# Performance work log

Measured on AMD Instinct MI355X. Metric: run time of the kernel, lower is better.

The kernel has to match this reference:

```python
import jax, jax.numpy as jnp
import numpy as np

EPS = 1e-5

def _conv1x1(x, w, b=None):
    # x: (B, Cin, H, W), w: (Cout, Cin) -> (B, Cout, H, W)
    y = jnp.einsum('bchw,oc->bohw', x, w)
    if b is not None:
        y = y + b[None, :, None, None]
    return y

def setup_inputs() -> dict:
    key = jax.random.key(0)
    ks = jax.random.split(key, 14)
    B, C, I = 4, 256, 128
    Ha = Wa = 64
    Hd = Wd = 128
    s = 0.05
    return {
        'detect':  jax.random.normal(ks[0], (B, C, Hd, Wd), jnp.float32),
        'aim':     jax.random.normal(ks[1], (B, C, Ha, Wa), jnp.float32),
        'g_w':     jax.random.normal(ks[2], (I, C), jnp.float32) * s,
        'g_b':     jax.random.normal(ks[3], (I,), jnp.float32) * s,
        'theta_w': jax.random.normal(ks[4], (I, C), jnp.float32) * s,
        'theta_b': jax.random.normal(ks[5], (I,), jnp.float32) * s,
        'phi_w':   jax.random.normal(ks[6], (I, C), jnp.float32) * s,
        'phi_b':   jax.random.normal(ks[7], (I,), jnp.float32) * s,
        'q_w':     jax.random.normal(ks[8], (C, I), jnp.float32) * s,
        'q_b':     jax.random.normal(ks[9], (C,), jnp.float32) * s,
        'bn_gamma': jax.random.normal(ks[10], (C,), jnp.float32),
        'bn_beta':  jax.random.normal(ks[11], (C,), jnp.float32),
        'bn_mean':  jax.random.normal(ks[12], (C,), jnp.float32),
        'bn_var':   jax.random.uniform(ks[13], (C,), jnp.float32) + 0.5,
    }

def reference(detect, aim, g_w, g_b, theta_w, theta_b, phi_w, phi_b,
              q_w, q_b, bn_gamma, bn_beta, bn_mean, bn_var):
    B, C, Hd, Wd = detect.shape
    _, _, Ha, Wa = aim.shape
    Na = Ha * Wa
    Nd = Hd * Wd
    I = g_w.shape[0]

    # 1x1 conv projections, flattened to token sequences
    a_g   = _conv1x1(aim, g_w, g_b).reshape(B, I, Na)        # g(aim)
    th_a  = _conv1x1(aim, theta_w, theta_b).reshape(B, I, Na)
    ph_d  = _conv1x1(detect, phi_w, phi_b).reshape(B, I, Nd)
    # (d_x = g(detect) is dead code in the original forward; omitted)

    # f = theta_x @ phi_x : (B, Na, Nd); permuted -> (B, Nd, Na); N = Na
    f = jnp.einsum('bia,bid->bad', th_a, ph_d)               # (B, Na, Nd)
    inv_n = jnp.float32(1.0 / Na)
    # non_det = (f^T / Na) @ a_x : (B, Nd, I) -> permute -> (B, I, Nd)
    non = jnp.einsum('bad,bia->bid', f * inv_n, a_g)         # (B, I, Nd)
    non = non.reshape(B, I, Hd, Wd)

    # Q: 1x1 conv (I -> C) + BatchNorm (inference mode, running stats)
    y = _conv1x1(non, q_w, q_b)
    inv_std = jax.lax.rsqrt(bn_var + EPS)
    y = (y - bn_mean[None, :, None, None]) * (bn_gamma * inv_std)[None, :, None, None] \
        + bn_beta[None, :, None, None]

    return y + detect
```

## Files before the change

### kernel.cpp

```cpp
#include <hip/hip_runtime.h>

constexpr int BB   = 4;
constexpr int CCH  = 256;
constexpr int IDIM = 128;
constexpr int NAa  = 4096;
constexpr int NDd  = 16384;
constexpr int PAD  = 320;
constexpr float NAinv = 1.0f / 4096.0f;

typedef __bf16 bf16x8 __attribute__((ext_vector_type(8)));
typedef float  f32x4  __attribute__((ext_vector_type(4)));

__device__ inline unsigned short f2bfu(float f) {
    unsigned u = __float_as_uint(f);
    u += 0x7FFFu + ((u >> 16) & 1u);
    return (unsigned short)(u >> 16);
}

__global__ __launch_bounds__(256) void k_prep(const float* __restrict__ qw,
                                              const float* __restrict__ gw,
                                              const float* __restrict__ gb,
                                              const float* __restrict__ thw,
                                              const float* __restrict__ thb,
                                              const float* __restrict__ phw,
                                              const float* __restrict__ phb,
                                              unsigned short* __restrict__ Ph,
                                              unsigned short* __restrict__ Rt) {
    const int idx = blockIdx.x * 256 + threadIdx.x;
    if (idx < CCH * PAD) {
        const int o = idx / PAD, c = idx - o * PAD;
        float acc = 0.f;
        if (c <= 256) {
            for (int i = 0; i < IDIM; ++i)
                acc += qw[o * IDIM + i] * ((c < 256) ? gw[i * CCH + c] : gb[i]);
        }
        Ph[idx] = f2bfu(acc);
    } else {
        const int id2 = idx - CCH * PAD;
        const int c2 = id2 / PAD, k = id2 - c2 * PAD;
        float acc = 0.f;
        if (k <= 256 && c2 <= 256) {
            for (int i = 0; i < IDIM; ++i) {
                const float av = (k < 256) ? thw[i * CCH + k] : thb[i];
                const float bv = (c2 < 256) ? phw[i * CCH + c2] : phb[i];
                acc += av * bv;
            }
        }
        Rt[id2] = f2bfu(acc);
    }
}

__device__ inline int at_idx(int row, int col) {
    return row * 320 + ((((col >> 3) ^ (row & 7)) << 3) | (col & 7));
}

__global__ __launch_bounds__(256) void k_V(const float* __restrict__ aim,
                                           const unsigned short* __restrict__ Ph,
                                           const unsigned short* __restrict__ Rt,
                                           unsigned short* __restrict__ V1,
                                           unsigned short* __restrict__ V2) {
    const int b = blockIdx.y, n0 = blockIdx.x * 64;
    const float* A = aim + (long)b * CCH * NAa;
    const int t = threadIdx.x, w = t >> 6, lane = t & 63, quad = lane >> 4, l16 = lane & 15;
    __shared__ __align__(16) unsigned short At[64 * 320];

    #pragma unroll 4
    for (int rep = 0; rep < 64; ++rep) {
        const int c = rep * 4 + w;
        At[at_idx(lane, c)] = f2bfu(A[(long)c * NAa + n0 + lane]);
    }
    {
        const int nn = t & 63, k0 = 256 + (t >> 6) * 16;
        #pragma unroll
        for (int k = k0; k < k0 + 16; ++k)
            At[at_idx(nn, k)] = (k == 256) ? (unsigned short)0x3F80u : (unsigned short)0u;
    }
    __syncthreads();

    for (int task = w; task < 9; task += 4) {
        const unsigned short* src;
        unsigned short* dst;
        int m0;
        if (task < 4) { m0 = task * 64;       src = Ph; dst = V1 + (long)b * CCH * NAa; }
        else          { m0 = (task - 4) * 64; src = Rt; dst = V2 + (long)b * PAD * NAa; }
        f32x4 acc[4][4] = {};
        for (int kt = 0; kt < PAD; kt += 32) {
            bf16x8 af[4], bfr[4];
            #pragma unroll
            for (int i = 0; i < 4; ++i)
                af[i] = *(const bf16x8*)(src + (long)(m0 + i * 16 + l16) * PAD + kt + quad * 8);
            #pragma unroll
            for (int j = 0; j < 4; ++j)
                bfr[j] = *(const bf16x8*)&At[at_idx(j * 16 + l16, kt + quad * 8)];
            #pragma unroll
            for (int i = 0; i < 4; ++i)
                #pragma unroll
                for (int j = 0; j < 4; ++j)
                    acc[i][j] = __builtin_amdgcn_mfma_f32_16x16x32_bf16(af[i], bfr[j], acc[i][j], 0, 0, 0);
        }
        #pragma unroll
        for (int i = 0; i < 4; ++i)
            #pragma unroll
            for (int j = 0; j < 4; ++j)
                #pragma unroll
                for (int reg = 0; reg < 4; ++reg)
                    dst[(long)(m0 + i * 16 + quad * 4 + reg) * NAa + n0 + j * 16 + l16] = f2bfu(acc[i][j][reg]);
    }
}

__global__ __launch_bounds__(256) void k_W(const unsigned short* __restrict__ V1,
                                           const unsigned short* __restrict__ V2,
                                           const float* __restrict__ qb,
                                           const float* __restrict__ gamma,
                                           const float* __restrict__ beta,
                                           const float* __restrict__ mean,
                                           const float* __restrict__ var,
                                           unsigned short* __restrict__ W5u,
                                           float* __restrict__ b5) {
    const int b = blockIdx.z;
    const int n0 = blockIdx.x * 64, m0 = blockIdx.y * 64;
    const unsigned short* Va = V1 + (long)b * CCH * NAa;
    const unsigned short* Vb = V2 + (long)b * PAD * NAa;
    const int t = threadIdx.x, w = t >> 6, lane = t & 63, quad = lane >> 4, l16 = lane & 15;
    __shared__ float sred[3 * 4096];

    f32x4 acc[4][4] = {};
    for (int ks = 0; ks < 32; ++ks) {
        const int k = w * 1024 + ks * 32 + quad * 8;
        bf16x8 af[4], bfr[4];
        #pragma unroll
        for (int i = 0; i < 4; ++i) af[i]  = *(const bf16x8*)(Va + (long)(m0 + i * 16 + l16) * NAa + k);
        #pragma unroll
        for (int j = 0; j < 4; ++j) bfr[j] = *(const bf16x8*)(Vb + (long)(n0 + j * 16 + l16) * NAa + k);
        #pragma unroll
        for (int i = 0; i < 4; ++i)
            #pragma unroll
            for (int j = 0; j < 4; ++j)
                acc[i][j] = __builtin_amdgcn_mfma_f32_16x16x32_bf16(af[i], bfr[j], acc[i][j], 0, 0, 0);
    }
    if (w > 0) {
        #pragma unroll
        for (int i = 0; i < 4; ++i)
            #pragma unroll
            for (int j = 0; j < 4; ++j)
                #pragma unroll
                for (int reg = 0; reg < 4; ++reg)
                    sred[(w - 1) * 4096 + ((i * 4 + j) * 4 + reg) * 64 + lane] = acc[i][j][reg];
    }
    __syncthreads();
    if (w == 0) {
        #pragma unroll
        for (int i = 0; i < 4; ++i)
            #pragma unroll
            for (int j = 0; j < 4; ++j)
                #pragma unroll
                for (int reg = 0; reg < 4; ++reg) {
                    float v = acc[i][j][reg];
                    #pragma unroll
                    for (int rg = 0; rg < 3; ++rg)
                        v += sred[rg * 4096 + ((i * 4 + j) * 4 + reg) * 64 + lane];
                    acc[i][j][reg] = v;
                }
        #pragma unroll
        for (int i = 0; i < 4; ++i) {
            #pragma unroll
            for (int reg = 0; reg < 4; ++reg) {
                const int o = m0 + i * 16 + quad * 4 + reg;
                const float s = gamma[o] * rsqrtf(var[o] + 1e-5f);
                #pragma unroll
                for (int j = 0; j < 4; ++j) {
                    const int c2 = n0 + j * 16 + l16;
                    const float val = acc[i][j][reg] * s * NAinv;
                    if (c2 < CCH)
                        W5u[((long)b * CCH + o) * CCH + c2] = f2bfu(val + (o == c2 ? 1.0f : 0.0f));
                    else if (c2 == CCH)
                        b5[b * CCH + o] = val + s * (qb[o] - mean[o]) + beta[o];
                }
            }
        }
    }
}

__global__ __launch_bounds__(512) void k_final(const float* __restrict__ D0,
                                               const unsigned short* __restrict__ W5u,
                                               const float* __restrict__ b5,
                                               float* __restrict__ out) {
    const int z = blockIdx.z;
    const int nb = blockIdx.x * 128;
    const float* D = D0 + (long)z * CCH * NDd;
    float* O = out + (long)z * CCH * NDd;
    const unsigned short* W = W5u + (long)z * CCH * CCH;
    const int t = threadIdx.x, wv = t >> 6, lane = t & 63, quad = lane >> 4, l16 = lane & 15;
    const int mw = (wv >> 1) * 64, nw = (wv & 1) * 64;
    const int r2 = t >> 4, g = t & 15;
    const bool st = (t < 256);
    __shared__ __align__(16) unsigned short lb[2][128][40];

    f32x4 xa[4], xb[4];
    bf16x8 af[2][4], bfr[4];

    auto load_tile = [&](f32x4* x, int kt) {
        const float* base = D + (long)(kt + 2 * r2) * NDd + nb + 8 * g;
        x[0] = *(const f32x4*)(base);
        x[1] = *(const f32x4*)(base + NDd);
        x[2] = *(const f32x4*)(base + 4);
        x[3] = *(const f32x4*)(base + NDd + 4);
    };
    auto write_tile = [&](int buf, const f32x4* x) {
        #pragma unroll
        for (int e2 = 0; e2 < 2; ++e2)
            #pragma unroll
            for (int c = 0; c < 4; ++c) {
                const int n = 8 * g + 4 * e2 + c;
                const int p = ((n & 7) << 4) + (n >> 3);
                const unsigned v = (unsigned)f2bfu(x[2 * e2][c]) |
                                   ((unsigned)f2bfu(x[2 * e2 + 1][c]) << 16);
                *(unsigned*)&lb[buf][p][2 * r2] = v;
            }
    };
    auto loadW = [&](bf16x8* a, int kt) {
        #pragma unroll
        for (int i = 0; i < 4; ++i)
            a[i] = *(const bf16x8*)(W + (long)(mw + i * 16 + l16) * CCH + kt + quad * 8);
    };

    int pj[4];
    #pragma unroll
    for (int j = 0; j < 4; ++j) {
        const int n = nw + j * 16 + l16;
        pj[j] = ((n & 7) << 4) + (n >> 3);
    }

    f32x4 acc[4][4] = {};
    if (st) { load_tile(xa, 0); load_tile(xb, 32); }
    loadW(af[0], 0);
    if (st) { write_tile(0, xa); load_tile(xa, 64); }
    #pragma unroll
    for (int it = 0; it < 8; ++it) {
        __syncthreads();
        const int kt = it * 32;
        #pragma unroll
        for (int j = 0; j < 4; ++j)
            bfr[j] = *(const bf16x8*)&lb[it & 1][pj[j]][quad * 8];
        #pragma unroll
        for (int i = 0; i < 4; ++i)
            #pragma unroll
            for (int j = 0; j < 4; ++j)
                acc[i][j] = __builtin_amdgcn_mfma_f32_16x16x32_bf16(af[it & 1][i], bfr[j], acc[i][j], 0, 0, 0);
        if (it < 7) {
            loadW(af[(it + 1) & 1], kt + 32);
            if (st) {
                write_tile((it + 1) & 1, (it & 1) ? xa : xb);
                if (it < 5) load_tile((it & 1) ? xa : xb, (it + 3) * 32);
            }
        }
    }
    #pragma unroll
    for (int i = 0; i < 4; ++i) {
        float bv[4];
        #pragma unroll
        for (int reg = 0; reg < 4; ++reg)
            bv[reg] = b5[z * CCH + mw + i * 16 + quad * 4 + reg];
        #pragma unroll
        for (int j = 0; j < 4; ++j) {
            const int n = nb + nw + j * 16 + l16;
            #pragma unroll
            for (int reg = 0; reg < 4; ++reg)
                O[(long)(mw + i * 16 + quad * 4 + reg) * NDd + n] = acc[i][j][reg] + bv[reg];
        }
    }
}

extern "C" void kernel_launch(void* const* d_in, const int* in_sizes, int n_in,
                              void* d_out, int out_size, void* d_ws, size_t ws_size,
                              hipStream_t stream) {
    const float* detect = (const float*)d_in[0];
    const float* aim    = (const float*)d_in[1];
    const float* g_w    = (const float*)d_in[2];
    const float* g_b    = (const float*)d_in[3];
    const float* th_w   = (const float*)d_in[4];
    const float* th_b   = (const float*)d_in[5];
    const float* phi_w  = (const float*)d_in[6];
    const float* phi_b  = (const float*)d_in[7];
    const float* q_w    = (const float*)d_in[8];
    const float* q_b    = (const float*)d_in[9];
    const float* gamma  = (const float*)d_in[10];
    const float* beta   = (const float*)d_in[11];
    const float* mean   = (const float*)d_in[12];
    const float* var    = (const float*)d_in[13];
    float* out = (float*)d_out;

    unsigned short* us = (unsigned short*)d_ws;
    unsigned short* V1u = us;
    unsigned short* V2u = V1u + 4194304;
    unsigned short* Phat_u  = V2u + 5242880;
    unsigned short* RhatT_u = Phat_u + 81920;
    unsigned short* W5u     = RhatT_u + 102400;
    float* b5 = (float*)(W5u + 262144);

    k_prep<<<dim3((CCH * PAD + PAD * PAD) / 256), dim3(256), 0, stream>>>(
        q_w, g_w, g_b, th_w, th_b, phi_w, phi_b, Phat_u, RhatT_u);
    k_V<<<dim3(NAa / 64, BB), dim3(256), 0, stream>>>(aim, Phat_u, RhatT_u, V1u, V2u);
    k_W<<<dim3(5, 4, BB), dim3(256), 0, stream>>>(V1u, V2u, q_b, gamma, beta, mean, var, W5u, b5);
    k_final<<<dim3(NDd / 128, 1, BB), dim3(512), 0, stream>>>(detect, W5u, b5, out);
}
```

Baseline: 240.2 us.

## Reassociate attention weight build through aim Gram matrix and fuse prep kernels

Replaces the per-batch projections V1/V2 over all Na tokens (then their contraction) with a Gram matrix S = aim·aimᵀ (256x256 per batch) plus aim row sums. The fused weight matrix is then rebuilt from small products Ph·S·Rtᵀ with rank-one bias corrections. Weight preparation, Gram and row-sum computation are merged into one launch. This removes the large bf16 intermediate writes and reads and one kernel launch. The cost is a serial small-GEMM chain in k2 that runs on only 16 blocks, and different bf16 rounding points.

```diff
diff --git a/kernel.cpp b/kernel.cpp
--- a/kernel.cpp
+++ b/kernel.cpp
@@ -16,166 +16,214 @@
     u += 0x7FFFu + ((u >> 16) & 1u);
     return (unsigned short)(u >> 16);
 }
-
-__global__ __launch_bounds__(256) void k_prep(const float* __restrict__ qw,
-                                              const float* __restrict__ gw,
-                                              const float* __restrict__ gb,
-                                              const float* __restrict__ thw,
-                                              const float* __restrict__ thb,
-                                              const float* __restrict__ phw,
-                                              const float* __restrict__ phb,
-                                              unsigned short* __restrict__ Ph,
-                                              unsigned short* __restrict__ Rt) {
-    const int idx = blockIdx.x * 256 + threadIdx.x;
-    if (idx < CCH * PAD) {
-        const int o = idx / PAD, c = idx - o * PAD;
-        float acc = 0.f;
-        if (c <= 256) {
-            for (int i = 0; i < IDIM; ++i)
-                acc += qw[o * IDIM + i] * ((c < 256) ? gw[i * CCH + c] : gb[i]);
-        }
-        Ph[idx] = f2bfu(acc);
-    } else {
-        const int id2 = idx - CCH * PAD;
-        const int c2 = id2 / PAD, k = id2 - c2 * PAD;
-        float acc = 0.f;
-        if (k <= 256 && c2 <= 256) {
-            for (int i = 0; i < IDIM; ++i) {
-                const float av = (k < 256) ? thw[i * CCH + k] : thb[i];
-                const float bv = (c2 < 256) ? phw[i * CCH + c2] : phb[i];
-                acc += av * bv;
-            }
-        }
-        Rt[id2] = f2bfu(acc);
-    }
-}
-
-__device__ inline int at_idx(int row, int col) {
-    return row * 320 + ((((col >> 3) ^ (row & 7)) << 3) | (col & 7));
-}
-
-__global__ __launch_bounds__(256) void k_V(const float* __restrict__ aim,
-                                           const unsigned short* __restrict__ Ph,
-                                           const unsigned short* __restrict__ Rt,
-                                           unsigned short* __restrict__ V1,
-                                           unsigned short* __restrict__ V2) {
-    const int b = blockIdx.y, n0 = blockIdx.x * 64;
-    const float* A = aim + (long)b * CCH * NAa;
-    const int t = threadIdx.x, w = t >> 6, lane = t & 63, quad = lane >> 4, l16 = lane & 15;
-    __shared__ __align__(16) unsigned short At[64 * 320];
-
-    #pragma unroll 4
-    for (int rep = 0; rep < 64; ++rep) {
-        const int c = rep * 4 + w;
-        At[at_idx(lane, c)] = f2bfu(A[(long)c * NAa + n0 + lane]);
-    }
-    {
-        const int nn = t & 63, k0 = 256 + (t >> 6) * 16;
-        #pragma unroll
-        for (int k = k0; k < k0 + 16; ++k)
-            At[at_idx(nn, k)] = (k == 256) ? (unsigned short)0x3F80u : (unsigned short)0u;
-    }
-    __syncthreads();
-
-    for (int task = w; task < 9; task += 4) {
-        const unsigned short* src;
-        unsigned short* dst;
-        int m0;
-        if (task < 4) { m0 = task * 64;       src = Ph; dst = V1 + (long)b * CCH * NAa; }
-        else          { m0 = (task - 4) * 64; src = Rt; dst = V2 + (long)b * PAD * NAa; }
+__device__ inline float bf2f(unsigned short u) {
+    return __uint_as_float((unsigned)u << 16);
+}
+__device__ inline bf16x8 ld_cvt8(const float* p) {
+    f32x4 a = *(const f32x4*)p;
+    f32x4 b = *(const f32x4*)(p + 4);
+    union { bf16x8 v; unsigned short u[8]; } t;
+    t.u[0] = f2bfu(a[0]); t.u[1] = f2bfu(a[1]); t.u[2] = f2bfu(a[2]); t.u[3] = f2bfu(a[3]);
+    t.u[4] = f2bfu(b[0]); t.u[5] = f2bfu(b[1]); t.u[6] = f2bfu(b[2]); t.u[7] = f2bfu(b[3]);
+    return t.v;
+}
+
+__global__ __launch_bounds__(256) void k1(const float* __restrict__ aim,
+                                          const float* __restrict__ qw,
+                                          const float* __restrict__ gw,
+                                          const float* __restrict__ gb,
+                                          const float* __restrict__ thw,
+                                          const float* __restrict__ thb,
+                                          const float* __restrict__ phw,
+                                          const float* __restrict__ phb,
+                                          unsigned short* __restrict__ Sg,
+                                          float* __restrict__ r,
+                                          unsigned short* __restrict__ Ph,
+                                          unsigned short* __restrict__ Rt) {
+    __shared__ __align__(16) char sm[49152];
+    const int bx = blockIdx.x, t = threadIdx.x;
+
+    if (bx < 64) {
+        const int b = bx >> 4, rem = bx & 15;
+        const int mb = (rem >> 2) * 64, nbb = (rem & 3) * 64;
+        const float* A = aim + (long)b * CCH * NAa;
+        const int w = t >> 6, lane = t & 63, quad = lane >> 4, l16 = lane & 15;
         f32x4 acc[4][4] = {};
-        for (int kt = 0; kt < PAD; kt += 32) {
+        for (int ks = 0; ks < 32; ++ks) {
+            const int k = w * 1024 + ks * 32 + quad * 8;
             bf16x8 af[4], bfr[4];
             #pragma unroll
-            for (int i = 0; i < 4; ++i)
-                af[i] = *(const bf16x8*)(src + (long)(m0 + i * 16 + l16) * PAD + kt + quad * 8);
-            #pragma unroll
-            for (int j = 0; j < 4; ++j)
-                bfr[j] = *(const bf16x8*)&At[at_idx(j * 16 + l16, kt + quad * 8)];
+            for (int i = 0; i < 4; ++i) af[i]  = ld_cvt8(A + (long)(mb + i * 16 + l16) * NAa + k);
+            #pragma unroll
+            for (int j = 0; j < 4; ++j) bfr[j] = ld_cvt8(A + (long)(nbb + j * 16 + l16) * NAa + k);
             #pragma unroll
             for (int i = 0; i < 4; ++i)
                 #pragma unroll
                 for (int j = 0; j < 4; ++j)
                     acc[i][j] = __builtin_amdgcn_mfma_f32_16x16x32_bf16(af[i], bfr[j], acc[i][j], 0, 0, 0);
         }
-        #pragma unroll
-        for (int i = 0; i < 4; ++i)
+        float* sred = (float*)sm;
+        if (w > 0) {
+            #pragma unroll
+            for (int i = 0; i < 4; ++i)
+                #pragma unroll
+                for (int j = 0; j < 4; ++j)
+                    #pragma unroll
+                    for (int reg = 0; reg < 4; ++reg)
+                        sred[(w - 1) * 4096 + ((i * 4 + j) * 4 + reg) * 64 + lane] = acc[i][j][reg];
+        }
+        __syncthreads();
+        if (w == 0) {
+            #pragma unroll
+            for (int i = 0; i < 4; ++i)
+                #pragma unroll
+                for (int j = 0; j < 4; ++j)
+                    #pragma unroll
+                    for (int reg = 0; reg < 4; ++reg) {
+                        float v = acc[i][j][reg];
+                        #pragma unroll
+                        for (int rg = 0; rg < 3; ++rg)
+                            v += sred[rg * 4096 + ((i * 4 + j) * 4 + reg) * 64 + lane];
+                        Sg[(long)b * 65536 + (long)(mb + i * 16 + quad * 4 + reg) * 256 + nbb + j * 16 + l16] = f2bfu(v);
+                    }
+        }
+    } else if (bx < 80) {
+        const int rid = bx - 64;
+        const int w = t >> 6, lane = t & 63;
+        for (int rr = 0; rr < 16; ++rr) {
+            const int row = rid * 64 + w * 16 + rr;
+            const float* src = aim + (long)row * NAa;
+            float s = 0.f;
+            #pragma unroll 4
+            for (int q = 0; q < 16; ++q) {
+                f32x4 v = *(const f32x4*)(src + q * 256 + lane * 4);
+                s += v[0] + v[1] + v[2] + v[3];
+            }
+            #pragma unroll
+            for (int off = 32; off > 0; off >>= 1) s += __shfl_down(s, off, 64);
+            if (lane == 0) r[row] = s;
+        }
+    } else {
+        const int idx = (bx - 80) * 256 + t;
+        if (idx < CCH * PAD) {
+            const int o = idx / PAD, c = idx - o * PAD;
+            float acc = 0.f;
+            if (c <= 256) {
+                for (int i = 0; i < IDIM; ++i)
+                    acc += qw[o * IDIM + i] * ((c < 256) ? gw[i * CCH + c] : gb[i]);
+            }
+            Ph[idx] = f2bfu(acc);
+        } else {
+            const int id2 = idx - CCH * PAD;
+            const int c2 = id2 / PAD, k = id2 - c2 * PAD;
+            float acc = 0.f;
+            if (k <= 256 && c2 <= 256) {
+                for (int i = 0; i < IDIM; ++i) {
+                    const float av = (k < 256) ? thw[i * CCH + k] : thb[i];
+                    const float bv = (c2 < 256) ? phw[i * CCH + c2] : phb[i];
+                    acc += av * bv;
+                }
+            }
+            Rt[id2] = f2bfu(acc);
+        }
+    }
+}
+
+__global__ __launch_bounds__(256) void k2(const unsigned short* __restrict__ Sg,
+                                          const float* __restrict__ r,
+                                          const unsigned short* __restrict__ Ph,
+                                          const unsigned short* __restrict__ Rt,
+                                          const float* __restrict__ qb,
+                                          const float* __restrict__ gamma,
+                                          const float* __restrict__ beta,
+                                          const float* __restrict__ mean,
+                                          const float* __restrict__ var,
+                                          unsigned short* __restrict__ W5u,
+                                          float* __restrict__ b5) {
+    const int b = blockIdx.y, m0 = blockIdx.x * 64;
+    const unsigned short* Sb = Sg + (long)b * 65536;
+    const float* rb = r + b * CCH;
+    const int t = threadIdx.x, w = t >> 6, lane = t & 63, quad = lane >> 4, l16 = lane & 15;
+    __shared__ __align__(16) unsigned short M1[64][264];
+    __shared__ float sv1[320], sv2[64];
+
+    for (int c2 = t; c2 < 320; c2 += 256) {
+        float s = 0.f;
+        for (int kk = 0; kk < 256; kk += 4) {
+            ushort4 u = *(const ushort4*)(Rt + (long)c2 * PAD + kk);
+            s += rb[kk] * bf2f(u.x) + rb[kk + 1] * bf2f(u.y) + rb[kk + 2] * bf2f(u.z) + rb[kk + 3] * bf2f(u.w);
+        }
+        sv1[c2] = s;
+    }
+    if (t < 64) {
+        const int o = m0 + t;
+        float s = 0.f;
+        for (int kk = 0; kk < 256; kk += 4) {
+            ushort4 u = *(const ushort4*)(Ph + (long)o * PAD + kk);
+            s += rb[kk] * bf2f(u.x) + rb[kk + 1] * bf2f(u.y) + rb[kk + 2] * bf2f(u.z) + rb[kk + 3] * bf2f(u.w);
+        }
+        sv2[t] = s;
+    }
+
+    {
+        f32x4 acc[4][4] = {};
+        for (int jt = 0; jt < 256; jt += 32) {
+            bf16x8 af[4], bfr[4];
+            #pragma unroll
+            for (int i = 0; i < 4; ++i)
+                af[i] = *(const bf16x8*)(Ph + (long)(m0 + i * 16 + l16) * PAD + jt + quad * 8);
             #pragma unroll
             for (int j = 0; j < 4; ++j)
+                bfr[j] = *(const bf16x8*)(Sb + (long)(w * 64 + j * 16 + l16) * 256 + jt + quad * 8);
+            #pragma unroll
+            for (int i = 0; i < 4; ++i)
+                #pragma unroll
+                for (int j = 0; j < 4; ++j)
+                    acc[i][j] = __builtin_amdgcn_mfma_f32_16x16x32_bf16(af[i], bfr[j], acc[i][j], 0, 0, 0);
+        }
+        #pragma unroll
+        for (int i = 0; i < 4; ++i)
+            #pragma unroll
+            for (int j = 0; j < 4; ++j)
                 #pragma unroll
                 for (int reg = 0; reg < 4; ++reg)
-                    dst[(long)(m0 + i * 16 + quad * 4 + reg) * NAa + n0 + j * 16 + l16] = f2bfu(acc[i][j][reg]);
-    }
-}
-
-__global__ __launch_bounds__(256) void k_W(const unsigned short* __restrict__ V1,
-                                           const unsigned short* __restrict__ V2,
-                                           const float* __restrict__ qb,
-                                           const float* __restrict__ gamma,
-                                           const float* __restrict__ beta,
-                                           const float* __restrict__ mean,
-                                           const float* __restrict__ var,
-                                           unsigned short* __restrict__ W5u,
-                                           float* __restrict__ b5) {
-    const int b = blockIdx.z;
-    const int n0 = blockIdx.x * 64, m0 = blockIdx.y * 64;
-    const unsigned short* Va = V1 + (long)b * CCH * NAa;
-    const unsigned short* Vb = V2 + (long)b * PAD * NAa;
-    const int t = threadIdx.x, w = t >> 6, lane = t & 63, quad = lane >> 4, l16 = lane & 15;
-    __shared__ float sred[3 * 4096];
-
-    f32x4 acc[4][4] = {};
-    for (int ks = 0; ks < 32; ++ks) {
-        const int k = w * 1024 + ks * 32 + quad * 8;
-        bf16x8 af[4], bfr[4];
-        #pragma unroll
-        for (int i = 0; i < 4; ++i) af[i]  = *(const bf16x8*)(Va + (long)(m0 + i * 16 + l16) * NAa + k);
-        #pragma unroll
-        for (int j = 0; j < 4; ++j) bfr[j] = *(const bf16x8*)(Vb + (long)(n0 + j * 16 + l16) * NAa + k);
-        #pragma unroll
-        for (int i = 0; i < 4; ++i)
-            #pragma unroll
-            for (int j = 0; j < 4; ++j)
+                    M1[i * 16 + quad * 4 + reg][w * 64 + j * 16 + l16] = f2bfu(acc[i][j][reg]);
+    }
+    __syncthreads();
+
+    f32x4 acc[4][5] = {};
+    for (int kt = 0; kt < 256; kt += 32) {
+        bf16x8 af[4], bfr[5];
+        #pragma unroll
+        for (int i = 0; i < 4; ++i)
+            af[i] = *(const bf16x8*)&M1[i * 16 + l16][kt + quad * 8];
+        #pragma unroll
+        for (int j = 0; j < 5; ++j)
+            bfr[j] = *(const bf16x8*)(Rt + (long)(w * 80 + j * 16 + l16) * PAD + kt + quad * 8);
+        #pragma unroll
+        for (int i = 0; i < 4; ++i)
+            #pragma unroll
+            for (int j = 0; j < 5; ++j)
                 acc[i][j] = __builtin_amdgcn_mfma_f32_16x16x32_bf16(af[i], bfr[j], acc[i][j], 0, 0, 0);
     }
-    if (w > 0) {
-        #pragma unroll
-        for (int i = 0; i < 4; ++i)
-            #pragma unroll
-            for (int j = 0; j < 4; ++j)
-                #pragma unroll
-                for (int reg = 0; reg < 4; ++reg)
-                    sred[(w - 1) * 4096 + ((i * 4 + j) * 4 + reg) * 64 + lane] = acc[i][j][reg];
-    }
-    __syncthreads();
-    if (w == 0) {
-        #pragma unroll
-        for (int i = 0; i < 4; ++i)
-            #pragma unroll
-            for (int j = 0; j < 4; ++j)
-                #pragma unroll
-                for (int reg = 0; reg < 4; ++reg) {
-                    float v = acc[i][j][reg];
-                    #pragma unroll
-                    for (int rg = 0; rg < 3; ++rg)
-                        v += sred[rg * 4096 + ((i * 4 + j) * 4 + reg) * 64 + lane];
-                    acc[i][j][reg] = v;
-                }
-        #pragma unroll
-        for (int i = 0; i < 4; ++i) {
-            #pragma unroll
-            for (int reg = 0; reg < 4; ++reg) {
-                const int o = m0 + i * 16 + quad * 4 + reg;
-                const float s = gamma[o] * rsqrtf(var[o] + 1e-5f);
-                #pragma unroll
-                for (int j = 0; j < 4; ++j) {
-                    const int c2 = n0 + j * 16 + l16;
-                    const float val = acc[i][j][reg] * s * NAinv;
-                    if (c2 < CCH)
-                        W5u[((long)b * CCH + o) * CCH + c2] = f2bfu(val + (o == c2 ? 1.0f : 0.0f));
-                    else if (c2 == CCH)
-                        b5[b * CCH + o] = val + s * (qb[o] - mean[o]) + beta[o];
-                }
+    #pragma unroll
+    for (int i = 0; i < 4; ++i) {
+        #pragma unroll
+        for (int reg = 0; reg < 4; ++reg) {
+            const int o = m0 + i * 16 + quad * 4 + reg;
+            const float ph256 = bf2f(Ph[(long)o * PAD + 256]);
+            const float s = gamma[o] * rsqrtf(var[o] + 1e-5f);
+            const float sv2v = sv2[i * 16 + quad * 4 + reg];
+            #pragma unroll
+            for (int j = 0; j < 5; ++j) {
+                const int c2 = w * 80 + j * 16 + l16;
+                const float rtc = bf2f(Rt[(long)c2 * PAD + 256]);
+                const float core = acc[i][j][reg] + ph256 * sv1[c2] + (sv2v + ph256 * 4096.0f) * rtc;
+                const float val = core * s * NAinv;
+                if (c2 < CCH)
+                    W5u[((long)b * CCH + o) * CCH + c2] = f2bfu(val + (o == c2 ? 1.0f : 0.0f));
+                else if (c2 == CCH)
+                    b5[b * CCH + o] = val + s * (qb[o] - mean[o]) + beta[o];
             }
         }
     }
@@ -291,16 +339,16 @@
     float* out = (float*)d_out;
 
     unsigned short* us = (unsigned short*)d_ws;
-    unsigned short* V1u = us;
-    unsigned short* V2u = V1u + 4194304;
-    unsigned short* Phat_u  = V2u + 5242880;
+    unsigned short* Sg      = us;
+    unsigned short* W5u     = Sg + 262144;
+    unsigned short* Phat_u  = W5u + 262144;
     unsigned short* RhatT_u = Phat_u + 81920;
-    unsigned short* W5u     = RhatT_u + 102400;
-    float* b5 = (float*)(W5u + 262144);
-
-    k_prep<<<dim3((CCH * PAD + PAD * PAD) / 256), dim3(256), 0, stream>>>(
-        q_w, g_w, g_b, th_w, th_b, phi_w, phi_b, Phat_u, RhatT_u);
-    k_V<<<dim3(NAa / 64, BB), dim3(256), 0, stream>>>(aim, Phat_u, RhatT_u, V1u, V2u);
-    k_W<<<dim3(5, 4, BB), dim3(256), 0, stream>>>(V1u, V2u, q_b, gamma, beta, mean, var, W5u, b5);
+    float* r  = (float*)(RhatT_u + 102400);
+    float* b5 = r + 1024;
+
+    k1<<<dim3(800), dim3(256), 0, stream>>>(aim, q_w, g_w, g_b, th_w, th_b, phi_w, phi_b,
+                                            Sg, r, Phat_u, RhatT_u);
+    k2<<<dim3(4, BB), dim3(256), 0, stream>>>(Sg, r, Phat_u, RhatT_u, q_b, gamma, beta,
+                                              mean, var, W5u, b5);
     k_final<<<dim3(NDd / 128, 1, BB), dim3(512), 0, stream>>>(detect, W5u, b5, out);
 }
```

Measured after the change: 251.2 us. 1.05x slower.
